# Optimization experiments

Hardware: AMD Instinct MI355X
Metric: run time of the kernel (lower is better)

Reference implementation:

```python
import jax, jax.numpy as jnp
import numpy as np

P_DROP = 0.009

def setup_inputs() -> dict:
    key = jax.random.key(0)
    kq, kk, kv, ks = jax.random.split(key, 4)
    B, S, D = 4, 4096, 64
    q = jax.random.normal(kq, (B, S, D), dtype=jnp.float32)
    k = jax.random.normal(kk, (B, S, D), dtype=jnp.float32)
    v = jax.random.normal(kv, (B, S, D), dtype=jnp.float32)
    s = jax.random.uniform(ks, (1,), dtype=jnp.float32) + 0.5  # positive scalar divisor
    return {"q": q, "k": k, "v": v, "s": s}

def reference(q, k, v, s):
    # qk = q @ k^T / s  -> [B, S, S]
    qk = jnp.einsum('bqd,bkd->bqk', q, k) / s[0]
    p = jax.nn.softmax(qk, axis=-1)
    # dropout p=0.009 (training mode in the original F.dropout); fixed key for determinism
    keep = 1.0 - P_DROP
    mask = jax.random.bernoulli(jax.random.key(1), keep, p.shape)
    p = jnp.where(mask, p / keep, jnp.zeros((), p.dtype))
    # output = dropout(softmax) @ v -> [B, S, Dv]
    return jnp.einsum('bqk,bkd->bqd', p, v)
```

## Files before the change

kernel.cpp:

```cpp
#include <hip/hip_runtime.h>
#include <stdint.h>

#define S_LEN 4096
#define KEEP_P 0.991f

typedef __attribute__((ext_vector_type(8)))  short bf16x8;
typedef __attribute__((ext_vector_type(16))) float f32x16;
typedef __attribute__((ext_vector_type(4)))  int   i32x4;
typedef __attribute__((ext_vector_type(2)))  int   i32x2;

static constexpr uint32_t KEEP_TH = 4256312832u;

__device__ __forceinline__ uint32_t rotl32(uint32_t x, uint32_t r) {
#if __has_builtin(__builtin_amdgcn_alignbit)
  return __builtin_amdgcn_alignbit(x, x, 32u - r);
#else
  return (x << r) | (x >> (32u - r));
#endif
}

__device__ __forceinline__ void threefry(uint32_t x0, uint32_t x1,
                                         uint32_t& o0, uint32_t& o1) {
  const uint32_t k0 = 0u, k1 = 1u, k2 = 0x1BD11BDBu;
  uint32_t v0 = x0 + k0, v1 = x1 + k1;
#define TFR(r) { v0 += v1; v1 = rotl32(v1, (r)); v1 ^= v0; }
  TFR(13) TFR(15) TFR(26) TFR(6)
  v0 += k1; v1 += k2 + 1u;
  TFR(17) TFR(29) TFR(16) TFR(24)
  v0 += k2; v1 += k0 + 2u;
  TFR(13) TFR(15) TFR(26) TFR(6)
  v0 += k0; v1 += k1 + 3u;
  TFR(17) TFR(29) TFR(16) TFR(24)
  v0 += k1; v1 += k2 + 4u;
  TFR(13) TFR(15) TFR(26) TFR(6)
  v0 += k2; v1 += k0 + 5u;
#undef TFR
  o0 = v0; o1 = v1;
}

__device__ __forceinline__ bool keep_partitionable(uint32_t i) {
  uint32_t o0, o1;
  threefry(0u, i, o0, o1);
  return (o0 ^ o1) < KEEP_TH;
}

__device__ __forceinline__ uint32_t f2u(float f){ union{float f;uint32_t u;}x; x.f=f; return x.u; }
__device__ __forceinline__ float u2f(uint32_t u){ union{uint32_t u;float f;}x; x.u=u; return x.f; }

__global__ __launch_bounds__(512, 2)
void attn_mfma(const float* __restrict__ Qg, const float* __restrict__ Kg,
               const float* __restrict__ Vg, const float* __restrict__ Sdiv,
               float* __restrict__ Out)
{
  __shared__ __align__(16) unsigned char smem[49152];
  __shared__ float sm_ml[2][3][2][32];
  char* khiB = (char*)smem;
  char* kloB = (char*)smem + 16384;
  char* vtsB = (char*)smem + 32768;
  float* smf = (float*)smem;

  const int t    = threadIdx.x;
  const int lane = t & 63;
  const int w    = t >> 6;
  const int wq   = w >> 2;
  const int h    = w & 3;
  const int l31  = lane & 31;
  const int hi5  = lane >> 5;

  const int blk = blockIdx.x;
  const int xcd = blk & 7;
  const int b   = xcd >> 1;
  const int qblock = ((xcd & 1) << 5) | (blk >> 3);
  const int qt  = qblock * 64;

  const float inv_s = 1.0f / Sdiv[0];
  const float* Qp = Qg + (size_t)b * S_LEN * 64;
  const float* Kp = Kg + (size_t)b * S_LEN * 64;
  const float* Vp = Vg + (size_t)b * S_LEN * 64;

#pragma unroll
  for (int rr = 0; rr < 2; ++rr) {
    int row = rr * 32 + (t >> 4);
    int c   = (t & 15) * 4;
    float4 q4 = *(const float4*)(Qp + (size_t)(qt + row) * 64 + c);
    uint32_t u0=f2u(q4.x),u1=f2u(q4.y),u2=f2u(q4.z),u3=f2u(q4.w);
    uint32_t h01=(u1&0xFFFF0000u)|(u0>>16), h23=(u3&0xFFFF0000u)|(u2>>16);
    uint32_t l0=f2u(q4.x-u2f(u0&0xFFFF0000u)), l1=f2u(q4.y-u2f(u1&0xFFFF0000u));
    uint32_t l2=f2u(q4.z-u2f(u2&0xFFFF0000u)), l3=f2u(q4.w-u2f(u3&0xFFFF0000u));
    uint32_t lo01=(l1&0xFFFF0000u)|(l0>>16), lo23=(l3&0xFFFF0000u)|(l2>>16);
    uint32_t off = ((uint32_t)(row*128 + c*2)) ^ ((uint32_t)((row&7)<<4));
    *(i32x2*)(khiB + off) = i32x2{(int)h01,(int)h23};
    *(i32x2*)(kloB + off) = i32x2{(int)lo01,(int)lo23};
  }
  __syncthreads();
  bf16x8 qhi[4], qlo[4];
  {
    int qrow = wq * 32 + l31;
#pragma unroll
    for (int kc = 0; kc < 4; ++kc) {
      uint32_t off = ((uint32_t)(qrow*128 + kc*32 + hi5*16)) ^ ((uint32_t)((qrow&7)<<4));
      qhi[kc] = *(const bf16x8*)(khiB + off);
      qlo[kc] = *(const bf16x8*)(kloB + off);
    }
  }
  __syncthreads();

  f32x16 o0, o1;
#pragma unroll
  for (int i = 0; i < 16; ++i) { o0[i] = 0.f; o1[i] = 0.f; }
  float m = -INFINITY, lsum = 0.f;

  const int rowk = h * 32 + l31;
  const uint32_t qglob = (uint32_t)(qt + wq * 32 + l31);
  const uint32_t fbrow = (((uint32_t)b * 4096u + qglob) * 4096u)
                       + (uint32_t)(h * 32) + 4u * (uint32_t)hi5;

  union PU { i32x4 i; bf16x8 bv; };

  for (int kt0 = 0; kt0 < S_LEN; kt0 += 128) {
#pragma unroll
    for (int rr = 0; rr < 4; ++rr) {
      int row = rr * 32 + (t >> 4);
      int c   = (t & 15) * 4;
      float4 k4 = *(const float4*)(Kp + (size_t)(kt0 + row) * 64 + c);
      uint32_t u0=f2u(k4.x),u1=f2u(k4.y),u2=f2u(k4.z),u3=f2u(k4.w);
      uint32_t h01=(u1&0xFFFF0000u)|(u0>>16), h23=(u3&0xFFFF0000u)|(u2>>16);
      uint32_t l0=f2u(k4.x-u2f(u0&0xFFFF0000u)), l1=f2u(k4.y-u2f(u1&0xFFFF0000u));
      uint32_t l2=f2u(k4.z-u2f(u2&0xFFFF0000u)), l3=f2u(k4.w-u2f(u3&0xFFFF0000u));
      uint32_t lo01=(l1&0xFFFF0000u)|(l0>>16), lo23=(l3&0xFFFF0000u)|(l2>>16);
      uint32_t off = ((uint32_t)(row*128 + c*2)) ^ ((uint32_t)((row&7)<<4));
      *(i32x2*)(khiB + off) = i32x2{(int)h01,(int)h23};
      *(i32x2*)(kloB + off) = i32x2{(int)lo01,(int)lo23};

      float4 v4 = *(const float4*)(Vp + (size_t)(kt0 + row) * 64 + c);
      uint32_t vp01, vp23;
      asm("v_cvt_pk_bf16_f32 %0, %1, %2" : "=v"(vp01) : "v"(v4.x), "v"(v4.y));
      asm("v_cvt_pk_bf16_f32 %0, %1, %2" : "=v"(vp23) : "v"(v4.z), "v"(v4.w));
      *(i32x2*)(vtsB + (uint32_t)(row*128 + c*2)) = i32x2{(int)vp01,(int)vp23};
    }
    __syncthreads();

    uint32_t mw = 0u;
    {
      const uint32_t fb = fbrow + (uint32_t)kt0;
#pragma unroll
      for (int p = 0; p < 4; ++p)
#pragma unroll
        for (int q = 0; q < 4; ++q) {
          uint32_t bitpos = (uint32_t)(8 * p + 4 * hi5 + q);
          mw |= (uint32_t)keep_partitionable(fb + (uint32_t)(8 * p + q)) << bitpos;
        }
    }

    f32x16 acc;
#pragma unroll
    for (int i = 0; i < 16; ++i) acc[i] = 0.f;
    bf16x8 kfrag[4];
    const uint32_t kswz = (uint32_t)((rowk&7)<<4);
#pragma unroll
    for (int kc = 0; kc < 4; ++kc) {
      uint32_t off = ((uint32_t)(rowk*128 + kc*32 + hi5*16)) ^ kswz;
      kfrag[kc] = *(const bf16x8*)(khiB + off);
    }
#pragma unroll
    for (int kc = 0; kc < 4; ++kc)
      acc = __builtin_amdgcn_mfma_f32_32x32x16_bf16(kfrag[kc], qhi[kc], acc, 0, 0, 0);
#pragma unroll
    for (int kc = 0; kc < 4; ++kc)
      acc = __builtin_amdgcn_mfma_f32_32x32x16_bf16(kfrag[kc], qlo[kc], acc, 0, 0, 0);
#pragma unroll
    for (int kc = 0; kc < 4; ++kc) {
      uint32_t off = ((uint32_t)(rowk*128 + kc*32 + hi5*16)) ^ kswz;
      kfrag[kc] = *(const bf16x8*)(kloB + off);
    }
#pragma unroll
    for (int kc = 0; kc < 4; ++kc)
      acc = __builtin_amdgcn_mfma_f32_32x32x16_bf16(kfrag[kc], qhi[kc], acc, 0, 0, 0);

    float z[16];
#pragma unroll
    for (int i = 0; i < 16; ++i) z[i] = acc[i] * inv_s;
    float tmax = z[0];
#pragma unroll
    for (int i = 1; i < 16; ++i) tmax = fmaxf(tmax, z[i]);
    tmax = fmaxf(tmax, __shfl_xor(tmax, 32));
    float mn = fmaxf(m, tmax);
    if (!__all(mn == m)) {
      float cr = __expf(m - mn);
      m = mn;
      lsum *= cr;
#pragma unroll
      for (int r = 0; r < 16; ++r) {
        int qr = (r & 3) + 8 * (r >> 2) + 4 * hi5;
        float cq = __shfl(cr, qr);
        o0[r] *= cq; o1[r] *= cq;
      }
    }
    float em[16];
#pragma unroll
    for (int r = 0; r < 16; ++r) {
      float e = __expf(z[r] - m);
      lsum += e;
      int bit = (r & 3) + 8 * (r >> 2) + 4 * hi5;
      em[r] = ((mw >> bit) & 1u) ? e : 0.f;
    }

    uint32_t cw[8];
#pragma unroll
    for (int i = 0; i < 8; ++i)
      asm("v_cvt_pk_bf16_f32 %0, %1, %2" : "=v"(cw[i]) : "v"(em[2*i]), "v"(em[2*i+1]));
    uint32_t sx[8];
#pragma unroll
    for (int i = 0; i < 8; ++i) sx[i] = (uint32_t)__shfl_xor((int)cw[i], 32);
    PU pf0, pf1;
    pf0.i = i32x4{ (int)(hi5 ? sx[2] : cw[0]),
                   (int)(hi5 ? sx[3] : cw[1]),
                   (int)(hi5 ? cw[2] : sx[0]),
                   (int)(hi5 ? cw[3] : sx[1]) };
    pf1.i = i32x4{ (int)(hi5 ? sx[6] : cw[4]),
                   (int)(hi5 ? sx[7] : cw[5]),
                   (int)(hi5 ? cw[6] : sx[4]),
                   (int)(hi5 ? cw[7] : sx[5]) };

    PU vf00, vf01, vf10, vf11;
#pragma unroll
    for (int ks = 0; ks < 2; ++ks)
#pragma unroll
      for (int vb = 0; vb < 2; ++vb) {
        int wds[4];
#pragma unroll
        for (int jj = 0; jj < 4; ++jj) {
          int k0 = 32*h + 16*ks + 8*hi5 + 2*jj;
          uint32_t lo = *(const uint16_t*)(vtsB + k0*128     + (vb*32 + l31)*2);
          uint32_t hi = *(const uint16_t*)(vtsB + (k0+1)*128 + (vb*32 + l31)*2);
          wds[jj] = (int)(lo | (hi << 16));
        }
        PU tmp; tmp.i = i32x4{wds[0], wds[1], wds[2], wds[3]};
        if (ks == 0 && vb == 0) vf00 = tmp;
        else if (ks == 0 && vb == 1) vf01 = tmp;
        else if (ks == 1 && vb == 0) vf10 = tmp;
        else vf11 = tmp;
      }

    o0 = __builtin_amdgcn_mfma_f32_32x32x16_bf16(pf0.bv, vf00.bv, o0, 0, 0, 0);
    o0 = __builtin_amdgcn_mfma_f32_32x32x16_bf16(pf1.bv, vf10.bv, o0, 0, 0, 0);
    o1 = __builtin_amdgcn_mfma_f32_32x32x16_bf16(pf0.bv, vf01.bv, o1, 0, 0, 0);
    o1 = __builtin_amdgcn_mfma_f32_32x32x16_bf16(pf1.bv, vf11.bv, o1, 0, 0, 0);
    __syncthreads();
  }

  lsum += __shfl_xor(lsum, 32);
  if (h > 0) {
    if (lane < 32) { sm_ml[wq][h-1][0][l31] = m; sm_ml[wq][h-1][1][l31] = lsum; }
    float* dst = smf + (size_t)(wq * 3 + (h - 1)) * 2048;
#pragma unroll
    for (int r = 0; r < 16; ++r) {
      int qr = (r & 3) + 8 * (r >> 2) + 4 * hi5;
      dst[qr * 64 + l31]      = o0[r];
      dst[qr * 64 + 32 + l31] = o1[r];
    }
  }
  __syncthreads();
  if (h == 0) {
#pragma unroll
    for (int hp = 1; hp < 4; ++hp) {
      float mp = sm_ml[wq][hp-1][0][l31];
      float lp = sm_ml[wq][hp-1][1][l31];
      float mm = fmaxf(m, mp);
      float ca = __expf(m - mm);
      float cb = __expf(mp - mm);
      lsum = lsum * ca + lp * cb;
      m = mm;
      const float* srcp = smf + (size_t)(wq * 3 + (hp - 1)) * 2048;
#pragma unroll
      for (int r = 0; r < 16; ++r) {
        int qr = (r & 3) + 8 * (r >> 2) + 4 * hi5;
        float caq = __shfl(ca, qr);
        float cbq = __shfl(cb, qr);
        o0[r] = o0[r] * caq + srcp[qr * 64 + l31] * cbq;
        o1[r] = o1[r] * caq + srcp[qr * 64 + 32 + l31] * cbq;
      }
    }
    float rinv = 1.0f / (lsum * KEEP_P);
    float* op = Out + ((size_t)b * S_LEN + (size_t)(qt + wq * 32)) * 64;
#pragma unroll
    for (int r = 0; r < 16; ++r) {
      int qr = (r & 3) + 8 * (r >> 2) + 4 * hi5;
      float rq = __shfl(rinv, qr);
      op[(size_t)qr * 64 + l31]      = o0[r] * rq;
      op[(size_t)qr * 64 + 32 + l31] = o1[r] * rq;
    }
  }
}

extern "C" void kernel_launch(void* const* d_in, const int* in_sizes, int n_in,
                              void* d_out, int out_size, void* d_ws, size_t ws_size,
                              hipStream_t stream) {
  (void)in_sizes; (void)n_in; (void)out_size; (void)d_ws; (void)ws_size;
  const float* q = (const float*)d_in[0];
  const float* k = (const float*)d_in[1];
  const float* v = (const float*)d_in[2];
  const float* s = (const float*)d_in[3];
  float* out = (float*)d_out;

  attn_mfma<<<dim3(256), dim3(512), 0, stream>>>(q, k, v, s, out);
}
```

Measured before the change: 201.8 us.

## Split KV sequence in two halves across blocks and merge partials

Doubles the grid by having each block handle half of the key/value range for a query tile, writing unnormalized bf16 partial outputs plus per-row max and sum to workspace. A second merge kernel combines the two halves with log-sum-exp rescaling and normalizes. Launch bounds rise to 4 blocks per CU. The aim is to fill all CUs, since 256 blocks underfill the device. The cost is an extra launch, workspace traffic, and bf16 rounding of partial outputs, which may hurt accuracy.

```diff
diff --git a/kernel.cpp b/kernel.cpp
--- a/kernel.cpp
+++ b/kernel.cpp
@@ -47,10 +47,10 @@
 __device__ __forceinline__ uint32_t f2u(float f){ union{float f;uint32_t u;}x; x.f=f; return x.u; }
 __device__ __forceinline__ float u2f(uint32_t u){ union{uint32_t u;float f;}x; x.u=u; return x.f; }
 
-__global__ __launch_bounds__(512, 2)
+__global__ __launch_bounds__(512, 4)
 void attn_mfma(const float* __restrict__ Qg, const float* __restrict__ Kg,
                const float* __restrict__ Vg, const float* __restrict__ Sdiv,
-               float* __restrict__ Out)
+               uint32_t* __restrict__ PartO, float* __restrict__ PartML)
 {
   __shared__ __align__(16) unsigned char smem[49152];
   __shared__ float sm_ml[2][3][2][32];
@@ -70,8 +70,11 @@
   const int blk = blockIdx.x;
   const int xcd = blk & 7;
   const int b   = xcd >> 1;
-  const int qblock = ((xcd & 1) << 5) | (blk >> 3);
-  const int qt  = qblock * 64;
+  const int i   = blk >> 3;
+  const int kvhalf = i & 1;
+  const int qtile  = ((xcd & 1) << 5) | (i >> 1);
+  const int qt  = qtile * 64;
+  const int kvbase = kvhalf * 2048;
 
   const float inv_s = 1.0f / Sdiv[0];
   const float* Qp = Qg + (size_t)b * S_LEN * 64;
@@ -107,7 +110,7 @@
 
   f32x16 o0, o1;
 #pragma unroll
-  for (int i = 0; i < 16; ++i) { o0[i] = 0.f; o1[i] = 0.f; }
+  for (int i2 = 0; i2 < 16; ++i2) { o0[i2] = 0.f; o1[i2] = 0.f; }
   float m = -INFINITY, lsum = 0.f;
 
   const int rowk = h * 32 + l31;
@@ -117,7 +120,7 @@
 
   union PU { i32x4 i; bf16x8 bv; };
 
-  for (int kt0 = 0; kt0 < S_LEN; kt0 += 128) {
+  for (int kt0 = kvbase; kt0 < kvbase + 2048; kt0 += 128) {
 #pragma unroll
     for (int rr = 0; rr < 4; ++rr) {
       int row = rr * 32 + (t >> 4);
@@ -154,7 +157,7 @@
 
     f32x16 acc;
 #pragma unroll
-    for (int i = 0; i < 16; ++i) acc[i] = 0.f;
+    for (int i2 = 0; i2 < 16; ++i2) acc[i2] = 0.f;
     bf16x8 kfrag[4];
     const uint32_t kswz = (uint32_t)((rowk&7)<<4);
 #pragma unroll
@@ -179,10 +182,10 @@
 
     float z[16];
 #pragma unroll
-    for (int i = 0; i < 16; ++i) z[i] = acc[i] * inv_s;
+    for (int i2 = 0; i2 < 16; ++i2) z[i2] = acc[i2] * inv_s;
     float tmax = z[0];
 #pragma unroll
-    for (int i = 1; i < 16; ++i) tmax = fmaxf(tmax, z[i]);
+    for (int i2 = 1; i2 < 16; ++i2) tmax = fmaxf(tmax, z[i2]);
     tmax = fmaxf(tmax, __shfl_xor(tmax, 32));
     float mn = fmaxf(m, tmax);
     if (!__all(mn == m)) {
@@ -207,11 +210,11 @@
 
     uint32_t cw[8];
 #pragma unroll
-    for (int i = 0; i < 8; ++i)
-      asm("v_cvt_pk_bf16_f32 %0, %1, %2" : "=v"(cw[i]) : "v"(em[2*i]), "v"(em[2*i+1]));
+    for (int i2 = 0; i2 < 8; ++i2)
+      asm("v_cvt_pk_bf16_f32 %0, %1, %2" : "=v"(cw[i2]) : "v"(em[2*i2]), "v"(em[2*i2+1]));
     uint32_t sx[8];
 #pragma unroll
-    for (int i = 0; i < 8; ++i) sx[i] = (uint32_t)__shfl_xor((int)cw[i], 32);
+    for (int i2 = 0; i2 < 8; ++i2) sx[i2] = (uint32_t)__shfl_xor((int)cw[i2], 32);
     PU pf0, pf1;
     pf0.i = i32x4{ (int)(hi5 ? sx[2] : cw[0]),
                    (int)(hi5 ? sx[3] : cw[1]),
@@ -281,27 +284,64 @@
         o1[r] = o1[r] * caq + srcp[qr * 64 + 32 + l31] * cbq;
       }
     }
-    float rinv = 1.0f / (lsum * KEEP_P);
-    float* op = Out + ((size_t)b * S_LEN + (size_t)(qt + wq * 32)) * 64;
+    if (lane < 32) {
+      PartML[blk * 128 +      (wq * 32 + l31)] = m;
+      PartML[blk * 128 + 64 + (wq * 32 + l31)] = lsum;
+    }
 #pragma unroll
     for (int r = 0; r < 16; ++r) {
       int qr = (r & 3) + 8 * (r >> 2) + 4 * hi5;
-      float rq = __shfl(rinv, qr);
-      op[(size_t)qr * 64 + l31]      = o0[r] * rq;
-      op[(size_t)qr * 64 + 32 + l31] = o1[r] * rq;
-    }
-  }
+      uint32_t pk;
+      asm("v_cvt_pk_bf16_f32 %0, %1, %2" : "=v"(pk) : "v"(o0[r]), "v"(o1[r]));
+      PartO[((size_t)blk * 64 + (size_t)(wq * 32 + qr)) * 32 + l31] = pk;
+    }
+  }
+}
+
+__global__ __launch_bounds__(256)
+void merge_kernel(const uint32_t* __restrict__ PartO, const float* __restrict__ PartML,
+                  float* __restrict__ Out)
+{
+  int tid = blockIdx.x * 256 + threadIdx.x;
+  int j   = tid & 31;
+  int row = tid >> 5;
+  int b   = row >> 12;
+  int qin = row & 4095;
+  int qtile = qin >> 6;
+  int rloc  = qin & 63;
+  int xcd = b * 2 + (qtile >> 5);
+  int ibase = (qtile & 31) << 1;
+  int blk0 = ((ibase + 0) << 3) | xcd;
+  int blk1 = ((ibase + 1) << 3) | xcd;
+
+  float m0 = PartML[blk0 * 128 + rloc], l0 = PartML[blk0 * 128 + 64 + rloc];
+  float m1 = PartML[blk1 * 128 + rloc], l1 = PartML[blk1 * 128 + 64 + rloc];
+  float mm = fmaxf(m0, m1);
+  float w0 = __expf(m0 - mm), w1 = __expf(m1 - mm);
+  float inv = 1.0f / ((l0 * w0 + l1 * w1) * KEEP_P);
+
+  uint32_t p0 = PartO[((size_t)blk0 * 64 + rloc) * 32 + j];
+  uint32_t p1 = PartO[((size_t)blk1 * 64 + rloc) * 32 + j];
+  float a_lo = u2f(p0 << 16),        b_lo = u2f(p1 << 16);
+  float a_hi = u2f(p0 & 0xFFFF0000u), b_hi = u2f(p1 & 0xFFFF0000u);
+
+  Out[(size_t)row * 64 + j]      = (a_lo * w0 + b_lo * w1) * inv;
+  Out[(size_t)row * 64 + j + 32] = (a_hi * w0 + b_hi * w1) * inv;
 }
 
 extern "C" void kernel_launch(void* const* d_in, const int* in_sizes, int n_in,
                               void* d_out, int out_size, void* d_ws, size_t ws_size,
                               hipStream_t stream) {
-  (void)in_sizes; (void)n_in; (void)out_size; (void)d_ws; (void)ws_size;
+  (void)in_sizes; (void)n_in; (void)out_size; (void)ws_size;
   const float* q = (const float*)d_in[0];
   const float* k = (const float*)d_in[1];
   const float* v = (const float*)d_in[2];
   const float* s = (const float*)d_in[3];
   float* out = (float*)d_out;
 
-  attn_mfma<<<dim3(256), dim3(512), 0, stream>>>(q, k, v, s, out);
-}
+  float*    part_ml = (float*)d_ws;
+  uint32_t* part_o  = (uint32_t*)((char*)d_ws + 512 * 128 * sizeof(float));
+
+  attn_mfma<<<dim3(512), dim3(512), 0, stream>>>(q, k, v, s, part_o, part_ml);
+  merge_kernel<<<dim3(2048), dim3(256), 0, stream>>>(part_o, part_ml, out);
+}
```

Measured after the change: 247.1 us. 22.4% more time.
